# Kernel optimization log

Hardware: AMD Instinct MI355X
Metric: run time of the kernel (lower is better)

## Reference

```python
import jax, jax.numpy as jnp
import numpy as np
from jax import lax

BS, EN, SEQ = 512, 512, 64
D_ENT, D_IN, D_KEY, D_F, H = 256, 1024, 32, 256, 32


def _layer_norm(x, g, b, eps=1e-5):
    m = x.mean(-1, keepdims=True)
    v = ((x - m) ** 2).mean(-1, keepdims=True)
    return (x - m) * lax.rsqrt(v + eps) * g + b


def setup_inputs() -> dict:
    key = jax.random.key(0)
    ks = jax.random.split(key, 24)
    f32 = jnp.float32

    def w(k, shape, fan_in):
        return (jax.random.normal(k, shape, dtype=f32) / np.sqrt(fan_in)).astype(f32)

    inp = {
        'entity_embedding': jax.random.normal(ks[0], (BS, EN, D_ENT), dtype=f32),
        'autoregressive_embedding': jax.random.normal(ks[1], (BS, D_IN), dtype=f32),
        'entity_num': jax.random.randint(ks[2], (BS,), 0, EN),
        'selected_units': jax.random.randint(ks[3], (BS, SEQ), 0, EN),
        'selected_units_num': jax.random.randint(ks[4], (BS,), 0, SEQ),
        # fc_block params (Linear: y = x @ W + b)
        'key_fc_w': w(ks[5], (D_ENT, D_KEY), D_ENT), 'key_fc_b': jnp.zeros((D_KEY,), f32),
        'q1_w': w(ks[6], (D_IN, D_F), D_IN), 'q1_b': jnp.zeros((D_F,), f32),
        'q2_w': w(ks[7], (D_F, D_KEY), D_F), 'q2_b': jnp.zeros((D_KEY,), f32),
        'e1_w': w(ks[8], (D_KEY, D_F), D_KEY), 'e1_b': jnp.zeros((D_F,), f32),
        'e2_w': w(ks[9], (D_F, D_IN), D_F), 'e2_b': jnp.zeros((D_IN,), f32),
        'end_embedding': jax.random.uniform(ks[10], (D_KEY,), dtype=f32,
                                            minval=-1.0 / np.sqrt(D_KEY), maxval=1.0 / np.sqrt(D_KEY)),
        # LayerNorm-LSTM (single layer), gate order: i, f, g, o
        'w_ih': w(ks[11], (D_KEY, 4 * H), D_KEY),
        'w_hh': w(ks[12], (H, 4 * H), H),
        'ln_ig': 1.0 + 0.1 * jax.random.normal(ks[13], (4 * H,), dtype=f32),
        'ln_ib': 0.1 * jax.random.normal(ks[14], (4 * H,), dtype=f32),
        'ln_hg': 1.0 + 0.1 * jax.random.normal(ks[15], (4 * H,), dtype=f32),
        'ln_hb': 0.1 * jax.random.normal(ks[16], (4 * H,), dtype=f32),
        'ln_cg': 1.0 + 0.1 * jax.random.normal(ks[17], (H,), dtype=f32),
        'ln_cb': 0.1 * jax.random.normal(ks[18], (H,), dtype=f32),
    }
    return inp


def _forward(entity_embedding, autoregressive_embedding, entity_num, selected_units,
             selected_units_num, key_fc_w, key_fc_b, q1_w, q1_b, q2_w, q2_b,
             e1_w, e1_b, e2_w, e2_b, end_embedding,
             w_ih, w_hh, ln_ig, ln_ib, ln_hg, ln_hb, ln_cg, ln_cb):
    bs = entity_embedding.shape[0]
    ar = jnp.arange(bs)
    # _get_key_mask: keys for all entities + zero pad slot, end_embedding at slot entity_num
    key = entity_embedding @ key_fc_w + key_fc_b                      # [bs, EN, Dk]
    key = jnp.concatenate([key, jnp.zeros((bs, 1, key.shape[-1]), key.dtype)], axis=1)  # [bs, EN+1, Dk]
    key = key.at[ar, entity_num].set(end_embedding.astype(key.dtype))
    key_embeddings = key                                              # reduce_type == 'selected_units_num'
    base_mask = jnp.arange(key.shape[1])[None, :] < (entity_num + 1)[:, None]  # sequence_mask(entity_num+1)
    mask0 = base_mask.at[ar, entity_num].set(False)                   # end token masked at step 0
    su_prev = jnp.concatenate([selected_units[:, :1], selected_units[:, :-1]], axis=1)

    def step(carry, xs):
        mask, ae, end_flag, one_hot, h, c = carry
        i, su_i, su_p = xs
        # teacher-forced mask evolution
        m1 = jnp.where(i == 1, mask.at[ar, entity_num].set(True), mask)
        m2 = m1.at[ar, su_p].set(False)
        mask = jnp.where(i > 0, m2, mask)
        # query_fc2(query_fc1(ae)) -> LN-LSTM cell
        x = jnp.maximum(ae @ q1_w + q1_b, 0.0) @ q2_w + q2_b
        gates = _layer_norm(x @ w_ih, ln_ig, ln_ib) + _layer_norm(h @ w_hh, ln_hg, ln_hb)
        ig, fg, cg, og = jnp.split(gates, 4, axis=-1)
        c = _layer_norm(jax.nn.sigmoid(fg) * c + jax.nn.sigmoid(ig) * jnp.tanh(cg), ln_cg, ln_cb)
        h = jax.nn.sigmoid(og) * jnp.tanh(c)
        # one-hot scatter of selected unit (skipped once end token seen)
        end_flag = end_flag | (su_i == entity_num)
        one_hot = one_hot.at[ar, su_i].max((~end_flag).astype(one_hot.dtype))
        # mean-pooled embedding of selected units -> embed_fc -> new ae
        emb = jnp.einsum('bn,bnd->bd', one_hot, key_embeddings)
        cnt = one_hot.sum(-1)
        denom = jnp.where((selected_units_num != 0) & (cnt > 0), cnt, 1.0)
        emb = emb / denom[:, None]
        ae = autoregressive_embedding + (jnp.maximum(emb @ e1_w + e1_b, 0.0) @ e2_w + e2_b)
        return (mask, ae, end_flag, one_hot, h, c), (h, mask)

    carry0 = (mask0, autoregressive_embedding,
              jnp.zeros((bs,), bool), jnp.zeros((bs, key.shape[1]), key.dtype),
              jnp.zeros((bs, w_hh.shape[0]), key.dtype), jnp.zeros((bs, w_hh.shape[0]), key.dtype))
    xs = (jnp.arange(selected_units.shape[1]), selected_units.T, su_prev.T)
    _, (queries, masks) = lax.scan(step, carry0, xs)   # [S,bs,Dk], [S,bs,EN+1]
    logits = jnp.einsum('sbd,bnd->sbn', queries, key)
    logits = jnp.where(masks, logits, jnp.asarray(-1e9, logits.dtype))
    return logits.transpose(1, 0, 2)                   # [bs, S, EN+1]


def reference(entity_embedding, autoregressive_embedding, entity_num, selected_units,
              selected_units_num, key_fc_w, key_fc_b, q1_w, q1_b, q2_w, q2_b,
              e1_w, e1_b, e2_w, e2_b, end_embedding,
              w_ih, w_hh, ln_ig, ln_ib, ln_hg, ln_hb, ln_cg, ln_cb):
    return _forward(entity_embedding, autoregressive_embedding, entity_num, selected_units,
                    selected_units_num, key_fc_w, key_fc_b, q1_w, q1_b, q2_w, q2_b,
                    e1_w, e1_b, e2_w, e2_b, end_embedding,
                    w_ih, w_hh, ln_ig, ln_ib, ln_hg, ln_hb, ln_cg, ln_cb)
```

## Files before the change

kernel.cpp:

```cpp
#include <hip/hip_runtime.h>
#include <cstdint>
#include <cstddef>


typedef short bf16x8 __attribute__((ext_vector_type(8)));
typedef float f32x4  __attribute__((ext_vector_type(4)));

__device__ __forceinline__ ushort f2bf(float f) {
    union { float f; unsigned u; } x; x.f = f;
    unsigned r = x.u + 0x7fffu + ((x.u >> 16) & 1u);
    return (ushort)(r >> 16);
}

__device__ __forceinline__ void gld16(const void* g, void* l) {
    __builtin_amdgcn_global_load_lds(
        (const __attribute__((address_space(1))) void*)g,
        (__attribute__((address_space(3))) void*)l,
        16, 0, 0);
}

template<int BM, int BN, int BK, int WR, int WC,
         bool RELU, bool ADDVEC, bool OUT_BF16, bool A_F32, bool KEYMODE>
__global__ __launch_bounds__(WR * WC * 64)
void mfma_gemm(const void* __restrict__ Av, int lda,
               const ushort* __restrict__ BT,
               const float* __restrict__ bias,
               const float* __restrict__ addvec, int ldadd,
               void* __restrict__ outv, int ldo,
               int K, int out_row_offset)
{
    constexpr int NT  = WR * WC * 64;
    constexpr int WM  = BM / WR, WN = BN / WC;
    constexpr int TMt = WM / 16, TNt = WN / 16;
    constexpr int KC  = BK / 8;
    constexpr int CHA = BM * KC, CHB = BN * KC;
    __shared__ __align__(16) ushort As[BM * BK];
    __shared__ __align__(16) ushort Bs[BN * BK];

    const int tid  = threadIdx.x;
    const int lane = tid & 63;
    const int w    = tid >> 6;
    const int wr   = w / WC, wc = w % WC;
    const int row0 = blockIdx.x * BM;
    const int n0   = blockIdx.y * BN;

    f32x4 acc[TMt][TNt];
#pragma unroll
    for (int i = 0; i < TMt; i++)
#pragma unroll
        for (int j = 0; j < TNt; j++)
#pragma unroll
            for (int r = 0; r < 4; r++) acc[i][j][r] = 0.f;

    const ushort* Ab = (const ushort*)Av;
    const float*  Af = (const float*)Av;

    for (int k0 = 0; k0 < K; k0 += BK) {
        if (A_F32) {
#pragma unroll
            for (int id = tid; id < CHA; id += NT) {
                int r = id / KC, kc = id % KC;
                const float* src = Af + (size_t)(row0 + r) * lda + k0 + kc * 8;
                float4 v0 = *(const float4*)(src);
                float4 v1 = *(const float4*)(src + 4);
                bf16x8 p;
                p[0] = (short)f2bf(v0.x); p[1] = (short)f2bf(v0.y);
                p[2] = (short)f2bf(v0.z); p[3] = (short)f2bf(v0.w);
                p[4] = (short)f2bf(v1.x); p[5] = (short)f2bf(v1.y);
                p[6] = (short)f2bf(v1.z); p[7] = (short)f2bf(v1.w);
                *(bf16x8*)(&As[id * 8]) = p;
            }
        } else {
#pragma unroll
            for (int id = tid; id < CHA; id += NT) {
                int r = id / KC, kc = id % KC;
                gld16(Ab + (size_t)(row0 + r) * lda + k0 + kc * 8, &As[id * 8]);
            }
        }
#pragma unroll
        for (int id = tid; id < CHB; id += NT) {
            int r = id / KC, kc = id % KC;
            gld16(BT + (size_t)(n0 + r) * K + k0 + kc * 8, &Bs[id * 8]);
        }
        __syncthreads();

        bf16x8 afr[TMt], bfr[TNt];
        const int krd = (lane >> 4) * 8;
        const int mrd = lane & 15;
#pragma unroll
        for (int tm = 0; tm < TMt; tm++)
            afr[tm] = *(bf16x8*)(&As[(wr * WM + tm * 16 + mrd) * BK + krd]);
#pragma unroll
        for (int tn = 0; tn < TNt; tn++)
            bfr[tn] = *(bf16x8*)(&Bs[(wc * WN + tn * 16 + mrd) * BK + krd]);
#pragma unroll
        for (int tm = 0; tm < TMt; tm++)
#pragma unroll
            for (int tn = 0; tn < TNt; tn++)
                acc[tm][tn] = __builtin_amdgcn_mfma_f32_16x16x32_bf16(
                    afr[tm], bfr[tn], acc[tm][tn], 0, 0, 0);
        __syncthreads();
    }

    float*  outf = (float*)outv;
    ushort* outh = (ushort*)outv;
    const int cn = lane & 15;
    const int rb = (lane >> 4) * 4;
#pragma unroll
    for (int tm = 0; tm < TMt; tm++) {
#pragma unroll
        for (int r = 0; r < 4; r++) {
            int grow = row0 + wr * WM + tm * 16 + rb + r;
            int b_   = grow & 511;
#pragma unroll
            for (int tn = 0; tn < TNt; tn++) {
                int gcol = n0 + wc * WN + tn * 16 + cn;
                float v = acc[tm][tn][r] + bias[gcol];
                if (RELU)   v = fmaxf(v, 0.f);
                if (ADDVEC) v += addvec[(size_t)b_ * ldadd + gcol];
                size_t oidx;
                if (KEYMODE) oidx = ((size_t)(grow >> 9) * 513 + b_) * 32 + gcol;
                else         oidx = (size_t)(grow + out_row_offset) * ldo + gcol;
                if (OUT_BF16) outh[oidx] = f2bf(v);
                else          outf[oidx] = v;
            }
        }
    }
}

__global__ __launch_bounds__(256) void misc_prep(
    const float* __restrict__ kw,  const float* __restrict__ e1w,
    const float* __restrict__ e2w, const float* __restrict__ q1w,
    const float* __restrict__ q2w,
    ushort* __restrict__ kwt,  ushort* __restrict__ e1wt,
    ushort* __restrict__ e2wt, ushort* __restrict__ q1wt,
    ushort* __restrict__ q2wt,
    const float* __restrict__ ar, ushort* __restrict__ AEb)
{
    int bx = blockIdx.x;
    if (bx < 512) {
        int i = (bx * 256 + threadIdx.x) * 4;
        float4 v = *(const float4*)(ar + i);
        ushort4 o;
        o.x = f2bf(v.x); o.y = f2bf(v.y); o.z = f2bf(v.z); o.w = f2bf(v.w);
        *(ushort4*)(AEb + i) = o;
        return;
    }
    bx -= 512;
    const float* W; ushort* WT; int K, N, t0;
    if      (bx < 8)   { W = kw;  WT = kwt;  K = 256;  N = 32;   t0 = bx; }
    else if (bx < 16)  { W = e1w; WT = e1wt; K = 32;   N = 256;  t0 = bx - 8; }
    else if (bx < 272) { W = e2w; WT = e2wt; K = 256;  N = 1024; t0 = bx - 16; }
    else if (bx < 528) { W = q1w; WT = q1wt; K = 1024; N = 256;  t0 = bx - 272; }
    else               { W = q2w; WT = q2wt; K = 256;  N = 32;   t0 = bx - 528; }
    int nn = N >> 5;
    int kt = (t0 / nn) * 32, nt = (t0 % nn) * 32;
    __shared__ float t[32][33];
    int x = threadIdx.x & 31, y = threadIdx.x >> 5;
    for (int i = y; i < 32; i += 8) t[i][x] = W[(size_t)(kt + i) * N + nt + x];
    __syncthreads();
    for (int i = y; i < 32; i += 8) WT[(size_t)(nt + i) * K + kt + x] = f2bf(t[x][i]);
}

__global__ __launch_bounds__(64) void prep_kernel(
    const int* __restrict__ en_g, const int* __restrict__ su_g,
    const int* __restrict__ sun_g, float* __restrict__ key,
    const float* __restrict__ eemb,
    int* __restrict__ fs_g, ushort* __restrict__ EMB)
{
    int b = blockIdx.x;
    int tid = threadIdx.x;
    __shared__ int fs_l[513];
    __shared__ int su_l[64];
    __shared__ float krows[64 * 32];
    for (int i = tid; i < 513; i += 64) fs_l[i] = 64;
    su_l[tid] = su_g[b * 64 + tid];
    int en = en_g[b];
    if (tid < 32) key[((size_t)b * 513 + 512) * 32 + tid] = 0.f;
    else          key[((size_t)b * 513 + en) * 32 + (tid - 32)] = eemb[tid - 32];
    __syncthreads();
    atomicMin(&fs_l[su_l[tid]], tid);
    unsigned long long ball = __ballot(su_l[tid] == en);
    int T = ball ? (__ffsll(ball) - 1) : 64;
    __syncthreads();
    {
        int d = tid & 31;
#pragma unroll 4
        for (int i = 0; i < 32; i++) {
            int r = 2 * i + (tid >> 5);
            krows[r * 32 + d] = key[((size_t)b * 513 + su_l[r]) * 32 + d];
        }
    }
    for (int i = tid; i < 513; i += 64) fs_g[(size_t)b * 513 + i] = fs_l[i];
    __syncthreads();

    int sun = sun_g[b];
    float a = 0.f;
    int cnt = 0;
    for (int i = 0; i < 64; i++) {
        bool nw = (i < T) && (fs_l[su_l[i]] == i);
        if (nw) {
            cnt++;
            if (tid < 32) a += krows[i * 32 + tid];
        }
        float denom = (sun != 0 && cnt > 0) ? (float)cnt : 1.0f;
        if (tid < 32) EMB[((size_t)i * 512 + b) * 32 + tid] = f2bf(a / denom);
    }
}

__device__ inline float sigm(float x) { return 1.0f / (1.0f + expf(-x)); }

__global__ __launch_bounds__(128) void lstm_kernel(
    const float* __restrict__ X, const float* __restrict__ wih_g,
    const float* __restrict__ whh_g,
    const float* __restrict__ lnig, const float* __restrict__ lnib,
    const float* __restrict__ lnhg, const float* __restrict__ lnhb,
    const float* __restrict__ lncg, const float* __restrict__ lncb,
    float* __restrict__ Q)
{
    const int wv = threadIdx.x >> 6;
    const int lane = threadIdx.x & 63;
    const int b = blockIdx.x * 2 + wv;
    __shared__ float xs[2][64 * 32];

    {
        int d = lane & 31;
#pragma unroll 8
        for (int i = 0; i < 32; i++) {
            int s = 2 * i + (lane >> 5);
            xs[wv][s * 32 + d] = X[((size_t)s * 512 + b) * 32 + d];
        }
    }
    float w0[32], w1[32], u0[32], u1[32];
#pragma unroll
    for (int k = 0; k < 32; k++) {
        w0[k] = wih_g[k * 128 + lane];
        w1[k] = wih_g[k * 128 + lane + 64];
        u0[k] = whh_g[k * 128 + lane];
        u1[k] = whh_g[k * 128 + lane + 64];
    }
    const float gi0 = lnig[lane], gi1 = lnig[lane + 64];
    const float bi0 = lnib[lane], bi1 = lnib[lane + 64];
    const float gh0 = lnhg[lane], gh1 = lnhg[lane + 64];
    const float bh0 = lnhb[lane], bh1 = lnhb[lane + 64];
    const int j = lane & 31;
    const float gc = lncg[j], bc = lncb[j];
    float h = 0.f, c = 0.f;
    __syncthreads();

    const float* xrow = &xs[wv][0];
    for (int s = 0; s < 64; s++) {
        float ax0 = 0.f, ax1 = 0.f, ah0 = 0.f, ah1 = 0.f;
#pragma unroll
        for (int k = 0; k < 32; k++) {
            float xk = xrow[s * 32 + k];
            float hk = __shfl(h, k);
            ax0 += xk * w0[k]; ax1 += xk * w1[k];
            ah0 += hk * u0[k]; ah1 += hk * u1[k];
        }
        float r0 = ax0 + ax1, r1 = ax0 * ax0 + ax1 * ax1;
        float r2 = ah0 + ah1, r3 = ah0 * ah0 + ah1 * ah1;
#pragma unroll
        for (int m = 1; m <= 32; m <<= 1) {
            r0 += __shfl_xor(r0, m); r1 += __shfl_xor(r1, m);
            r2 += __shfl_xor(r2, m); r3 += __shfl_xor(r3, m);
        }
        float mx = r0 * (1.f / 128.f), vx = r1 * (1.f / 128.f) - mx * mx;
        float mh = r2 * (1.f / 128.f), vh = r3 * (1.f / 128.f) - mh * mh;
        float sx = rsqrtf(vx + 1e-5f), sh = rsqrtf(vh + 1e-5f);
        float g0 = (ax0 - mx) * sx * gi0 + bi0 + (ah0 - mh) * sh * gh0 + bh0;
        float g1 = (ax1 - mx) * sx * gi1 + bi1 + (ah1 - mh) * sh * gh1 + bh1;
        float igv = __shfl(g0, j),      fgv = __shfl(g0, j + 32);
        float cgv = __shfl(g1, j),      ogv = __shfl(g1, j + 32);
        float cc = sigm(fgv) * c + sigm(igv) * tanhf(cgv);
        float s0 = cc, s1 = cc * cc;
#pragma unroll
        for (int m = 1; m <= 32; m <<= 1) {
            s0 += __shfl_xor(s0, m); s1 += __shfl_xor(s1, m);
        }
        float mc = s0 * (1.f / 64.f), vc = s1 * (1.f / 64.f) - mc * mc;
        c = (cc - mc) * rsqrtf(vc + 1e-5f) * gc + bc;
        h = sigm(ogv) * tanhf(c);
        if (lane < 32) Q[((size_t)b * 64 + s) * 32 + lane] = h;
    }
}

__global__ __launch_bounds__(128) void logits_kernel(
    const float* __restrict__ key, const float* __restrict__ Q,
    const int* __restrict__ fs_g, const int* __restrict__ en_g,
    float* __restrict__ out)
{
    int b = blockIdx.x;
    int n0 = blockIdx.y * 128;
    int tid = threadIdx.x;
    __shared__ float Qs[64 * 32];
    __shared__ float Ks[128 * 33];
    for (int i = tid * 4; i < 2048; i += 512)
        *(float4*)(&Qs[i]) = *(const float4*)(Q + (size_t)b * 2048 + i);
    for (int i = tid; i < 4096; i += 128) {
        int r = i >> 5, d = i & 31;
        int n = n0 + r;
        Ks[r * 33 + d] = (n < 513) ? key[((size_t)b * 513 + n) * 32 + d] : 0.f;
    }
    __syncthreads();
    int n = n0 + tid;
    if (n < 513) {
        int en = en_g[b];
        int f = fs_g[(size_t)b * 513 + n];
        float kreg[32];
#pragma unroll
        for (int d = 0; d < 32; d++) kreg[d] = Ks[tid * 33 + d];
        for (int s = 0; s < 64; s++) {
            float a = 0.f;
#pragma unroll
            for (int d = 0; d < 32; d++) a += Qs[s * 32 + d] * kreg[d];
            bool m = (s == 0) ? (n < en) : ((n <= en) && (f >= s));
            out[((size_t)b * 64 + s) * 513 + n] = m ? a : -1e9f;
        }
    }
}

extern "C" void kernel_launch(void* const* d_in, const int* in_sizes, int n_in,
                              void* d_out, int out_size, void* d_ws, size_t ws_size,
                              hipStream_t stream)
{
    const float* ee   = (const float*)d_in[0];
    const float* ar   = (const float*)d_in[1];
    const int*   en   = (const int*)d_in[2];
    const int*   su   = (const int*)d_in[3];
    const int*   sun  = (const int*)d_in[4];
    const float* kw   = (const float*)d_in[5];
    const float* kb   = (const float*)d_in[6];
    const float* q1w  = (const float*)d_in[7];
    const float* q1b  = (const float*)d_in[8];
    const float* q2w  = (const float*)d_in[9];
    const float* q2b  = (const float*)d_in[10];
    const float* e1w  = (const float*)d_in[11];
    const float* e1b  = (const float*)d_in[12];
    const float* e2w  = (const float*)d_in[13];
    const float* e2b  = (const float*)d_in[14];
    const float* eemb = (const float*)d_in[15];
    const float* wih  = (const float*)d_in[16];
    const float* whh  = (const float*)d_in[17];
    const float* lnig = (const float*)d_in[18];
    const float* lnib = (const float*)d_in[19];
    const float* lnhg = (const float*)d_in[20];
    const float* lnhb = (const float*)d_in[21];
    const float* lncg = (const float*)d_in[22];
    const float* lncb = (const float*)d_in[23];
    float* outp = (float*)d_out;

    char* p = (char*)d_ws;
    float*  key  = (float*)p;  p += (size_t)512 * 513 * 32 * 4;
    ushort* AEb  = (ushort*)p; p += (size_t)32768 * 1024 * 2;
    ushort* Z1b  = (ushort*)p; p += (size_t)32768 * 256 * 2;
    ushort* EMBb = (ushort*)p; p += (size_t)32768 * 32 * 2;
    float*  X    = (float*)p;  p += (size_t)32768 * 32 * 4;
    float*  Q    = (float*)p;  p += (size_t)32768 * 32 * 4;
    int*    fs   = (int*)p;    p += (size_t)512 * 513 * 4;
    ushort* kwt  = (ushort*)p; p += (size_t)32 * 256 * 2;
    ushort* e1wt = (ushort*)p; p += (size_t)256 * 32 * 2;
    ushort* e2wt = (ushort*)p; p += (size_t)1024 * 256 * 2;
    ushort* q1wt = (ushort*)p; p += (size_t)256 * 1024 * 2;
    ushort* q2wt = (ushort*)p; p += (size_t)32 * 256 * 2;

    misc_prep<<<1048, 256, 0, stream>>>(kw, e1w, e2w, q1w, q2w,
                                        kwt, e1wt, e2wt, q1wt, q2wt, ar, AEb);

    mfma_gemm<128, 32, 32, 4, 1, false, false, false, true, true>
        <<<dim3(2048, 1), 256, 0, stream>>>(ee, 256, kwt, kb, nullptr, 0, key, 32, 256, 0);
    prep_kernel<<<512, 64, 0, stream>>>(en, su, sun, key, eemb, fs, EMBb);

    mfma_gemm<128, 128, 32, 2, 2, true, false, true, false, false>
        <<<dim3(252, 2), 256, 0, stream>>>(EMBb, 32, e1wt, e1b, nullptr, 0, Z1b, 256, 32, 0);
    mfma_gemm<128, 128, 32, 2, 2, false, true, true, false, false>
        <<<dim3(252, 8), 256, 0, stream>>>(Z1b, 256, e2wt, e2b, ar, 1024, AEb, 1024, 256, 512);
    mfma_gemm<128, 128, 32, 2, 2, true, false, true, false, false>
        <<<dim3(256, 2), 256, 0, stream>>>(AEb, 1024, q1wt, q1b, nullptr, 0, Z1b, 256, 1024, 0);
    mfma_gemm<128, 32, 32, 4, 1, false, false, false, false, false>
        <<<dim3(256, 1), 256, 0, stream>>>(Z1b, 256, q2wt, q2b, nullptr, 0, X, 32, 256, 0);

    lstm_kernel<<<256, 128, 0, stream>>>(X, wih, whh, lnig, lnib, lnhg, lnhb, lncg, lncb, Q);

    logits_kernel<<<dim3(512, 5), 128, 0, stream>>>(key, Q, fs, en, outp);
}
```

Before: 701.8 us.

## Fuse e1/e2 and q1/q2 MLP GEMM pairs via LDS, store keys as bf16

The two back-to-back MLP GEMM pairs (e1→e2 with the residual add, and q1→q2) each become a single kernel. The ReLU'd intermediate of 128 rows × 256 stays in LDS instead of making a round trip through global memory, and the q1 stage uses a larger 128×256 tile with BK=64. The key tensor is also stored as bf16 instead of fp32, which halves the traffic for the key write, the gather and the logits reads. The costs are heavy LDS use that limits each CU to one block, an unpipelined single-buffered load loop, and a small precision loss in the keys used for the logits.

```diff
diff --git a/kernel.cpp b/kernel.cpp
--- a/kernel.cpp
+++ b/kernel.cpp
@@ -10,6 +10,9 @@
     union { float f; unsigned u; } x; x.f = f;
     unsigned r = x.u + 0x7fffu + ((x.u >> 16) & 1u);
     return (ushort)(r >> 16);
+}
+__device__ __forceinline__ float bf2f(ushort u) {
+    union { unsigned u; float f; } x; x.u = ((unsigned)u) << 16; return x.f;
 }
 
 __device__ __forceinline__ void gld16(const void* g, void* l) {
@@ -20,14 +23,12 @@
 }
 
 template<int BM, int BN, int BK, int WR, int WC,
-         bool RELU, bool ADDVEC, bool OUT_BF16, bool A_F32, bool KEYMODE>
+         bool RELU, bool OUT_BF16, bool A_F32, bool KEYMODE>
 __global__ __launch_bounds__(WR * WC * 64)
 void mfma_gemm(const void* __restrict__ Av, int lda,
                const ushort* __restrict__ BT,
                const float* __restrict__ bias,
-               const float* __restrict__ addvec, int ldadd,
-               void* __restrict__ outv, int ldo,
-               int K, int out_row_offset)
+               void* __restrict__ outv, int ldo, int K)
 {
     constexpr int NT  = WR * WC * 64;
     constexpr int WM  = BM / WR, WN = BN / WC;
@@ -116,16 +117,226 @@
             for (int tn = 0; tn < TNt; tn++) {
                 int gcol = n0 + wc * WN + tn * 16 + cn;
                 float v = acc[tm][tn][r] + bias[gcol];
-                if (RELU)   v = fmaxf(v, 0.f);
-                if (ADDVEC) v += addvec[(size_t)b_ * ldadd + gcol];
+                if (RELU) v = fmaxf(v, 0.f);
                 size_t oidx;
                 if (KEYMODE) oidx = ((size_t)(grow >> 9) * 513 + b_) * 32 + gcol;
-                else         oidx = (size_t)(grow + out_row_offset) * ldo + gcol;
+                else         oidx = (size_t)grow * ldo + gcol;
                 if (OUT_BF16) outh[oidx] = f2bf(v);
                 else          outf[oidx] = v;
             }
         }
     }
+}
+
+__global__ __launch_bounds__(256, 1) void fused_e(
+    const ushort* __restrict__ EMB, const ushort* __restrict__ e1wt,
+    const float* __restrict__ e1b, const ushort* __restrict__ e2wt,
+    const float* __restrict__ e2b, const float* __restrict__ ar,
+    ushort* __restrict__ AEb)
+{
+    __shared__ __align__(16) ushort Z1s[128 * 256];
+    __shared__ __align__(16) char  Stage[64 * 1024];
+    ushort* As  = (ushort*)Stage;
+    ushort* Bs1 = (ushort*)(Stage + 8 * 1024);
+    ushort* Bs2 = (ushort*)Stage;
+
+    const int tid  = threadIdx.x;
+    const int lane = tid & 63;
+    const int w    = tid >> 6;
+    const int wr   = w >> 1, wc = w & 1;
+    const int row0 = blockIdx.x * 128;
+    const int mrd  = lane & 15;
+    const int krd  = (lane >> 4) * 8;
+    const int cn   = lane & 15;
+    const int rb   = (lane >> 4) * 4;
+
+#pragma unroll
+    for (int id = tid; id < 512; id += 256)
+        gld16(EMB + (size_t)(row0 + id / 4) * 32 + (id % 4) * 8, &As[id * 8]);
+#pragma unroll
+    for (int id = tid; id < 1024; id += 256)
+        gld16(e1wt + (size_t)(id / 4) * 32 + (id % 4) * 8, &Bs1[id * 8]);
+    __syncthreads();
+
+    bf16x8 afr[4];
+#pragma unroll
+    for (int tm = 0; tm < 4; tm++)
+        afr[tm] = *(bf16x8*)(&As[(wr * 64 + tm * 16 + mrd) * 32 + krd]);
+#pragma unroll
+    for (int nc1 = 0; nc1 < 2; nc1++) {
+        f32x4 acc[4][4];
+#pragma unroll
+        for (int tm = 0; tm < 4; tm++)
+#pragma unroll
+            for (int tn = 0; tn < 4; tn++) {
+                bf16x8 bfr = *(bf16x8*)(&Bs1[(nc1 * 128 + wc * 64 + tn * 16 + mrd) * 32 + krd]);
+                f32x4 z; z[0]=0.f; z[1]=0.f; z[2]=0.f; z[3]=0.f;
+                acc[tm][tn] = __builtin_amdgcn_mfma_f32_16x16x32_bf16(afr[tm], bfr, z, 0, 0, 0);
+            }
+#pragma unroll
+        for (int tm = 0; tm < 4; tm++)
+#pragma unroll
+            for (int r = 0; r < 4; r++) {
+                int row = wr * 64 + tm * 16 + rb + r;
+#pragma unroll
+                for (int tn = 0; tn < 4; tn++) {
+                    int col = nc1 * 128 + wc * 64 + tn * 16 + cn;
+                    Z1s[row * 256 + col] = f2bf(fmaxf(acc[tm][tn][r] + e1b[col], 0.f));
+                }
+            }
+    }
+    __syncthreads();
+
+    for (int nc = 0; nc < 8; nc++) {
+#pragma unroll
+        for (int id = tid; id < 4096; id += 256)
+            gld16(e2wt + (size_t)(nc * 128 + id / 32) * 256 + (id % 32) * 8, &Bs2[id * 8]);
+        __syncthreads();
+        f32x4 acc[4][4];
+#pragma unroll
+        for (int tm = 0; tm < 4; tm++)
+#pragma unroll
+            for (int tn = 0; tn < 4; tn++)
+#pragma unroll
+                for (int r = 0; r < 4; r++) acc[tm][tn][r] = 0.f;
+#pragma unroll
+        for (int kk = 0; kk < 256; kk += 32) {
+            bf16x8 af[4], bf[4];
+#pragma unroll
+            for (int tm = 0; tm < 4; tm++)
+                af[tm] = *(bf16x8*)(&Z1s[(wr * 64 + tm * 16 + mrd) * 256 + kk + krd]);
+#pragma unroll
+            for (int tn = 0; tn < 4; tn++)
+                bf[tn] = *(bf16x8*)(&Bs2[(wc * 64 + tn * 16 + mrd) * 256 + kk + krd]);
+#pragma unroll
+            for (int tm = 0; tm < 4; tm++)
+#pragma unroll
+                for (int tn = 0; tn < 4; tn++)
+                    acc[tm][tn] = __builtin_amdgcn_mfma_f32_16x16x32_bf16(
+                        af[tm], bf[tn], acc[tm][tn], 0, 0, 0);
+        }
+        __syncthreads();
+#pragma unroll
+        for (int tm = 0; tm < 4; tm++)
+#pragma unroll
+            for (int r = 0; r < 4; r++) {
+                int grow = row0 + wr * 64 + tm * 16 + rb + r;
+                int b_   = grow & 511;
+#pragma unroll
+                for (int tn = 0; tn < 4; tn++) {
+                    int col = nc * 128 + wc * 64 + tn * 16 + cn;
+                    float v = acc[tm][tn][r] + e2b[col] + ar[(size_t)b_ * 1024 + col];
+                    AEb[(size_t)(512 + grow) * 1024 + col] = f2bf(v);
+                }
+            }
+    }
+}
+
+__global__ __launch_bounds__(256, 1) void fused_q(
+    const ushort* __restrict__ AEb, const ushort* __restrict__ q1wt,
+    const float* __restrict__ q1b, const ushort* __restrict__ q2wt,
+    const float* __restrict__ q2b, float* __restrict__ X)
+{
+    __shared__ __align__(16) ushort Y1s[128 * 256];
+    __shared__ __align__(16) char  Stage[48 * 1024];
+    ushort* As  = (ushort*)Stage;
+    ushort* Bs  = (ushort*)(Stage + 16 * 1024);
+    ushort* Bs2 = (ushort*)Stage;
+
+    const int tid  = threadIdx.x;
+    const int lane = tid & 63;
+    const int w    = tid >> 6;
+    const int wr   = w >> 1, wc = w & 1;
+    const int row0 = blockIdx.x * 128;
+    const int mrd  = lane & 15;
+    const int krd  = (lane >> 4) * 8;
+    const int cn   = lane & 15;
+    const int rb   = (lane >> 4) * 4;
+
+    f32x4 acc[4][8];
+#pragma unroll
+    for (int tm = 0; tm < 4; tm++)
+#pragma unroll
+        for (int tn = 0; tn < 8; tn++)
+#pragma unroll
+            for (int r = 0; r < 4; r++) acc[tm][tn][r] = 0.f;
+
+    for (int k0 = 0; k0 < 1024; k0 += 64) {
+#pragma unroll
+        for (int id = tid; id < 1024; id += 256)
+            gld16(AEb + (size_t)(row0 + id / 8) * 1024 + k0 + (id % 8) * 8, &As[id * 8]);
+#pragma unroll
+        for (int id = tid; id < 2048; id += 256)
+            gld16(q1wt + (size_t)(id / 8) * 1024 + k0 + (id % 8) * 8, &Bs[id * 8]);
+        __syncthreads();
+#pragma unroll
+        for (int kk = 0; kk < 64; kk += 32) {
+            bf16x8 af[4], bf[8];
+#pragma unroll
+            for (int tm = 0; tm < 4; tm++)
+                af[tm] = *(bf16x8*)(&As[(wr * 64 + tm * 16 + mrd) * 64 + kk + krd]);
+#pragma unroll
+            for (int tn = 0; tn < 8; tn++)
+                bf[tn] = *(bf16x8*)(&Bs[(wc * 128 + tn * 16 + mrd) * 64 + kk + krd]);
+#pragma unroll
+            for (int tm = 0; tm < 4; tm++)
+#pragma unroll
+                for (int tn = 0; tn < 8; tn++)
+                    acc[tm][tn] = __builtin_amdgcn_mfma_f32_16x16x32_bf16(
+                        af[tm], bf[tn], acc[tm][tn], 0, 0, 0);
+        }
+        __syncthreads();
+    }
+#pragma unroll
+    for (int tm = 0; tm < 4; tm++)
+#pragma unroll
+        for (int r = 0; r < 4; r++) {
+            int row = wr * 64 + tm * 16 + rb + r;
+#pragma unroll
+            for (int tn = 0; tn < 8; tn++) {
+                int col = wc * 128 + tn * 16 + cn;
+                Y1s[row * 256 + col] = f2bf(fmaxf(acc[tm][tn][r] + q1b[col], 0.f));
+            }
+        }
+#pragma unroll
+    for (int id = tid; id < 1024; id += 256)
+        gld16(q2wt + (size_t)(id / 32) * 256 + (id % 32) * 8, &Bs2[id * 8]);
+    __syncthreads();
+
+    f32x4 a2[2][2];
+#pragma unroll
+    for (int tm = 0; tm < 2; tm++)
+#pragma unroll
+        for (int tn = 0; tn < 2; tn++)
+#pragma unroll
+            for (int r = 0; r < 4; r++) a2[tm][tn][r] = 0.f;
+#pragma unroll
+    for (int kk = 0; kk < 256; kk += 32) {
+        bf16x8 af[2], bf[2];
+#pragma unroll
+        for (int tm = 0; tm < 2; tm++)
+            af[tm] = *(bf16x8*)(&Y1s[(w * 32 + tm * 16 + mrd) * 256 + kk + krd]);
+#pragma unroll
+        for (int tn = 0; tn < 2; tn++)
+            bf[tn] = *(bf16x8*)(&Bs2[(tn * 16 + mrd) * 256 + kk + krd]);
+#pragma unroll
+        for (int tm = 0; tm < 2; tm++)
+#pragma unroll
+            for (int tn = 0; tn < 2; tn++)
+                a2[tm][tn] = __builtin_amdgcn_mfma_f32_16x16x32_bf16(
+                    af[tm], bf[tn], a2[tm][tn], 0, 0, 0);
+    }
+#pragma unroll
+    for (int tm = 0; tm < 2; tm++)
+#pragma unroll
+        for (int r = 0; r < 4; r++) {
+            int grow = row0 + w * 32 + tm * 16 + rb + r;
+#pragma unroll
+            for (int tn = 0; tn < 2; tn++) {
+                int col = tn * 16 + cn;
+                X[(size_t)grow * 32 + col] = a2[tm][tn][r] + q2b[col];
+            }
+        }
 }
 
 __global__ __launch_bounds__(256) void misc_prep(
@@ -164,7 +375,7 @@
 
 __global__ __launch_bounds__(64) void prep_kernel(
     const int* __restrict__ en_g, const int* __restrict__ su_g,
-    const int* __restrict__ sun_g, float* __restrict__ key,
+    const int* __restrict__ sun_g, ushort* __restrict__ key,
     const float* __restrict__ eemb,
     int* __restrict__ fs_g, ushort* __restrict__ EMB)
 {
@@ -176,8 +387,8 @@
     for (int i = tid; i < 513; i += 64) fs_l[i] = 64;
     su_l[tid] = su_g[b * 64 + tid];
     int en = en_g[b];
-    if (tid < 32) key[((size_t)b * 513 + 512) * 32 + tid] = 0.f;
-    else          key[((size_t)b * 513 + en) * 32 + (tid - 32)] = eemb[tid - 32];
+    if (tid < 32) key[((size_t)b * 513 + 512) * 32 + tid] = 0;
+    else          key[((size_t)b * 513 + en) * 32 + (tid - 32)] = f2bf(eemb[tid - 32]);
     __syncthreads();
     atomicMin(&fs_l[su_l[tid]], tid);
     unsigned long long ball = __ballot(su_l[tid] == en);
@@ -188,7 +399,7 @@
 #pragma unroll 4
         for (int i = 0; i < 32; i++) {
             int r = 2 * i + (tid >> 5);
-            krows[r * 32 + d] = key[((size_t)b * 513 + su_l[r]) * 32 + d];
+            krows[r * 32 + d] = bf2f(key[((size_t)b * 513 + su_l[r]) * 32 + d]);
         }
     }
     for (int i = tid; i < 513; i += 64) fs_g[(size_t)b * 513 + i] = fs_l[i];
@@ -222,7 +433,6 @@
     const int lane = threadIdx.x & 63;
     const int b = blockIdx.x * 2 + wv;
     __shared__ float xs[2][64 * 32];
-
     {
         int d = lane & 31;
 #pragma unroll 8
@@ -286,7 +496,7 @@
 }
 
 __global__ __launch_bounds__(128) void logits_kernel(
-    const float* __restrict__ key, const float* __restrict__ Q,
+    const ushort* __restrict__ key, const float* __restrict__ Q,
     const int* __restrict__ fs_g, const int* __restrict__ en_g,
     float* __restrict__ out)
 {
@@ -297,10 +507,16 @@
     __shared__ float Ks[128 * 33];
     for (int i = tid * 4; i < 2048; i += 512)
         *(float4*)(&Qs[i]) = *(const float4*)(Q + (size_t)b * 2048 + i);
-    for (int i = tid; i < 4096; i += 128) {
-        int r = i >> 5, d = i & 31;
+    for (int g = tid; g < 1024; g += 128) {
+        int e = g * 4, r = e >> 5, d = e & 31;
         int n = n0 + r;
-        Ks[r * 33 + d] = (n < 513) ? key[((size_t)b * 513 + n) * 32 + d] : 0.f;
+        if (n < 513) {
+            ushort4 k4 = *(const ushort4*)(key + ((size_t)b * 513 + n) * 32 + d);
+            Ks[r * 33 + d + 0] = bf2f(k4.x);
+            Ks[r * 33 + d + 1] = bf2f(k4.y);
+            Ks[r * 33 + d + 2] = bf2f(k4.z);
+            Ks[r * 33 + d + 3] = bf2f(k4.w);
+        }
     }
     __syncthreads();
     int n = n0 + tid;
@@ -351,9 +567,8 @@
     float* outp = (float*)d_out;
 
     char* p = (char*)d_ws;
-    float*  key  = (float*)p;  p += (size_t)512 * 513 * 32 * 4;
+    ushort* key  = (ushort*)p; p += (size_t)512 * 513 * 32 * 2;
     ushort* AEb  = (ushort*)p; p += (size_t)32768 * 1024 * 2;
-    ushort* Z1b  = (ushort*)p; p += (size_t)32768 * 256 * 2;
     ushort* EMBb = (ushort*)p; p += (size_t)32768 * 32 * 2;
     float*  X    = (float*)p;  p += (size_t)32768 * 32 * 4;
     float*  Q    = (float*)p;  p += (size_t)32768 * 32 * 4;
@@ -367,18 +582,12 @@
     misc_prep<<<1048, 256, 0, stream>>>(kw, e1w, e2w, q1w, q2w,
                                         kwt, e1wt, e2wt, q1wt, q2wt, ar, AEb);
 
-    mfma_gemm<128, 32, 32, 4, 1, false, false, false, true, true>
-        <<<dim3(2048, 1), 256, 0, stream>>>(ee, 256, kwt, kb, nullptr, 0, key, 32, 256, 0);
+    mfma_gemm<128, 32, 32, 4, 1, false, true, true, true>
+        <<<dim3(2048, 1), 256, 0, stream>>>(ee, 256, kwt, kb, key, 32, 256);
     prep_kernel<<<512, 64, 0, stream>>>(en, su, sun, key, eemb, fs, EMBb);
 
-    mfma_gemm<128, 128, 32, 2, 2, true, false, true, false, false>
-        <<<dim3(252, 2), 256, 0, stream>>>(EMBb, 32, e1wt, e1b, nullptr, 0, Z1b, 256, 32, 0);
-    mfma_gemm<128, 128, 32, 2, 2, false, true, true, false, false>
-        <<<dim3(252, 8), 256, 0, stream>>>(Z1b, 256, e2wt, e2b, ar, 1024, AEb, 1024, 256, 512);
-    mfma_gemm<128, 128, 32, 2, 2, true, false, true, false, false>
-        <<<dim3(256, 2), 256, 0, stream>>>(AEb, 1024, q1wt, q1b, nullptr, 0, Z1b, 256, 1024, 0);
-    mfma_gemm<128, 32, 32, 4, 1, false, false, false, false, false>
-        <<<dim3(256, 1), 256, 0, stream>>>(Z1b, 256, q2wt, q2b, nullptr, 0, X, 32, 256, 0);
+    fused_e<<<252, 256, 0, stream>>>(EMBb, e1wt, e1b, e2wt, e2b, ar, AEb);
+    fused_q<<<256, 256, 0, stream>>>(AEb, q1wt, q1b, q2wt, q2b, X);
 
     lstm_kernel<<<256, 128, 0, stream>>>(X, wih, whh, lnig, lnib, lnhg, lnhb, lncg, lncb, Q);
 
```

Result: slower. 799.5 us (+13.9%).
